# Kernel optimization log

Measured on AMD Instinct MI355X. Metric: run time of the kernel, lower is better.

The kernel has to match this reference:

```python
import jax, jax.numpy as jnp
import numpy as np

B, T, D = 16, 2048, 256

def setup_inputs() -> dict:
    key = jax.random.key(0)
    k1, k2, k3 = jax.random.split(key, 3)
    q = jax.random.normal(k1, (B, T, D), dtype=jnp.float32)
    a = jax.random.normal(k2, (B, T, D), dtype=jnp.float32)
    # original uses 'uniform' init; scale ~ small
    U = jax.random.uniform(k3, (D, D), dtype=jnp.float32, minval=-0.05, maxval=0.05)
    return {"q": q, "a": a, "U": U}

def reference(q, a, U):
    # G[b,i,j] = tanh( (q[b,i,:] @ U) . a[b,j,:] )
    qU = jnp.einsum('btd,de->bte', q, U)                 # [B,Tq,D]
    G = jnp.tanh(jnp.einsum('btd,bsd->bts', qU, a))      # [B,Tq,Ta]
    g_q = jax.nn.softmax(jnp.max(G, axis=-1), axis=1)    # [B,Tq]
    g_a = jax.nn.softmax(jnp.max(G, axis=1), axis=1)     # [B,Ta]
    q_out = jnp.einsum('btd,bt->bd', q, g_q)             # [B,D]
    a_out = jnp.einsum('bsd,bs->bd', a, g_a)             # [B,D]
    return (q_out, a_out)
```

## Files before the change

### kernel.cpp

```cpp
#include <hip/hip_runtime.h>
#include <stdint.h>

typedef __attribute__((ext_vector_type(8))) short s8v;
typedef __attribute__((ext_vector_type(4))) float f4v;

__device__ __forceinline__ unsigned short f2bf(float f) {
  unsigned u = __float_as_uint(f);
  u = u + 0x7FFFu + ((u >> 16) & 1u);
  return (unsigned short)(u >> 16);
}
__device__ __forceinline__ unsigned encf(float f) {
  unsigned i = __float_as_uint(f);
  return (i & 0x80000000u) ? ~i : (i | 0x80000000u);
}
__device__ __forceinline__ float decf(unsigned u) {
  unsigned i = (u & 0x80000000u) ? (u & 0x7FFFFFFFu) : ~u;
  return __uint_as_float(i);
}
__device__ __forceinline__ void gload_lds16(const unsigned short* g, unsigned short* l) {
  __builtin_amdgcn_global_load_lds((const __attribute__((address_space(1))) void*)g,
                                   (__attribute__((address_space(3))) void*)l, 16, 0, 0);
}

__global__ void convert_kernel(const float4* __restrict__ q, const float4* __restrict__ a,
                               const float* __restrict__ U,
                               ushort4* __restrict__ qb, ushort4* __restrict__ ab,
                               unsigned short* __restrict__ Ut,
                               unsigned* __restrict__ rcmax, float* __restrict__ out) {
  const int bx = blockIdx.x;
  if (bx < 8192) {
    const int i = bx * 256 + threadIdx.x;
    float4 v = q[i];
    qb[i] = make_ushort4(f2bf(v.x), f2bf(v.y), f2bf(v.z), f2bf(v.w));
    float4 w = a[i];
    ab[i] = make_ushort4(f2bf(w.x), f2bf(w.y), f2bf(w.z), f2bf(w.w));
  } else if (bx < 8256) {
    const int idx = (bx - 8192) * 256 + threadIdx.x;
    const int n  = idx >> 6;
    const int k4 = (idx & 63) * 4;
    ushort4 o;
    o.x = f2bf(U[(k4 + 0) * 256 + n]);
    o.y = f2bf(U[(k4 + 1) * 256 + n]);
    o.z = f2bf(U[(k4 + 2) * 256 + n]);
    o.w = f2bf(U[(k4 + 3) * 256 + n]);
    *(ushort4*)&Ut[n * 256 + k4] = o;
  } else if (bx < 8320) {
    const int idx = (bx - 8256) * 256 + threadIdx.x;
    *(uint4*)&rcmax[idx * 4] = make_uint4(0u, 0u, 0u, 0u);
  } else {
    out[(bx - 8320) * 256 + threadIdx.x] = 0.f;
  }
}

__global__ __attribute__((amdgpu_flat_work_group_size(512, 512), amdgpu_waves_per_eu(2, 2)))
void fused_qu_smax(const unsigned short* __restrict__ qb,
                   const unsigned short* __restrict__ Ut,
                   const unsigned short* __restrict__ ab,
                   unsigned* __restrict__ rowmax,
                   unsigned* __restrict__ colmax) {
  extern __shared__ char smem[];
  unsigned short* qUs    = (unsigned short*)smem;
  unsigned short* Bs2    = (unsigned short*)(smem + 65536);
  unsigned*       colLds = (unsigned*)(smem + 131072);
  unsigned*       rowLds = (unsigned*)(smem + 139264);
#define SBUF(k) ((unsigned short*)(smem + ((k) << 15)))

  const int tid = threadIdx.x;
  const int b = blockIdx.x, tm = blockIdx.y;

  const int lane = tid & 63;
  const int m16  = lane & 15;
  const int quad = lane >> 4;
  const int wave = tid >> 6;
  const int wm   = wave >> 2;
  const int wn   = wave & 3;
  const int wr32 = (wave >> 1) * 32;
  const int wc32 = (wave & 1) * 32;
  const int srow = tid >> 3;
  const int scol = (((tid & 7) ^ (srow & 7))) * 8;

  #pragma unroll
  for (int i = 0; i < 4; ++i) colLds[i * 512 + tid] = 0u;
  if (tid < 128) rowLds[tid] = 0u;

  const unsigned short* Ab_ = ab + (long)b * 2048 * 256;

#define STG64(tb, dst) do {                                                    \
    _Pragma("unroll")                                                          \
    for (int e_ = 0; e_ < 4; ++e_) {                                           \
      const int u_ = e_ * 512 + tid;         \
      const int row_ = u_ >> 5;                                                \
      const int chs_ = (u_ & 31) ^ (row_ & 7);                                 \
      gload_lds16(Ab_ + (long)((tb) * 64 + row_) * 256 + chs_ * 8,             \
                  &(dst)[u_ * 8]);                                             \
    }                                                                          \
  } while (0)

  const unsigned short* Aq = qb + ((long)b * 2048 + tm * 128) * 256;
  {
    f4v acc[4][4] = {};

#define STAGE1(kt, dst) do {                                                   \
    const int k0_ = (kt) * 64;                                                 \
    _Pragma("unroll")                                                          \
    for (int i_ = 0; i_ < 2; ++i_)                                             \
      gload_lds16(Aq + (long)(i_ * 64 + srow) * 256 + k0_ + scol,              \
                  &(dst)[i_ * 4096 + tid * 8]);                                \
    _Pragma("unroll")                                                          \
    for (int i_ = 0; i_ < 4; ++i_)                                             \
      gload_lds16(Ut + (long)(i_ * 64 + srow) * 256 + k0_ + scol,              \
                  &(dst)[8192 + i_ * 4096 + tid * 8]);                         \
  } while (0)

#define COMPUTE1(buf) do {                                                     \
    _Pragma("unroll")                                                          \
    for (int kk_ = 0; kk_ < 2; ++kk_) {                                        \
      const int cs_ = ((kk_ * 4 + quad) ^ (m16 & 7)) * 8;                      \
      s8v af_[4], bf_[4];                                                      \
      _Pragma("unroll")                                                        \
      for (int i_ = 0; i_ < 4; ++i_)                                           \
        af_[i_] = *(const s8v*)&(buf)[(wm * 64 + i_ * 16 + m16) * 64 + cs_];   \
      _Pragma("unroll")                                                        \
      for (int j_ = 0; j_ < 4; ++j_)                                           \
        bf_[j_] = *(const s8v*)&(buf)[8192 + (wn * 64 + j_ * 16 + m16) * 64 + cs_]; \
      _Pragma("unroll")                                                        \
      for (int i_ = 0; i_ < 4; ++i_)                                           \
        _Pragma("unroll")                                                      \
        for (int j_ = 0; j_ < 4; ++j_)                                         \
          acc[i_][j_] = __builtin_amdgcn_mfma_f32_16x16x32_bf16(af_[i_], bf_[j_], acc[i_][j_], 0, 0, 0); \
    }                                                                          \
  } while (0)

    STAGE1(0, Bs2);
    STAGE1(1, qUs);
    asm volatile("s_waitcnt vmcnt(6)" ::: "memory");
    __builtin_amdgcn_s_barrier();
    COMPUTE1(Bs2);
    __builtin_amdgcn_s_barrier();
    STAGE1(2, Bs2);
    asm volatile("s_waitcnt vmcnt(6)" ::: "memory");
    __builtin_amdgcn_s_barrier();
    COMPUTE1(qUs);
    __builtin_amdgcn_s_barrier();
    STAGE1(3, qUs);
    asm volatile("s_waitcnt vmcnt(6)" ::: "memory");
    __builtin_amdgcn_s_barrier();
    COMPUTE1(Bs2);
    asm volatile("s_waitcnt vmcnt(0)" ::: "memory");
    __builtin_amdgcn_s_barrier();
    STG64(0, SBUF(2));
    STG64(1, SBUF(3));
    COMPUTE1(qUs);
    asm volatile("s_waitcnt lgkmcnt(0)" ::: "memory");
    __builtin_amdgcn_s_barrier();

    #pragma unroll
    for (int i = 0; i < 4; ++i)
      #pragma unroll
      for (int r = 0; r < 4; ++r) {
        const int lr = wm * 64 + i * 16 + quad * 4 + r;
        #pragma unroll
        for (int j = 0; j < 4; ++j) {
          const int col = wn * 64 + j * 16 + m16;
          const int ch = (col >> 3) ^ (lr & 7);
          qUs[lr * 256 + ch * 8 + (col & 7)] = f2bf(acc[i][j][r]);
        }
      }
  }
  asm volatile("s_waitcnt lgkmcnt(0)" ::: "memory");
  __builtin_amdgcn_s_barrier();

  s8v aq[2][8];
  #pragma unroll
  for (int kq = 0; kq < 8; ++kq) {
    const int cs = ((kq * 4 + quad) ^ (m16 & 7)) * 8;
    aq[0][kq] = *(const s8v*)&qUs[(wr32 + m16) * 256 + cs];
    aq[1][kq] = *(const s8v*)&qUs[(wr32 + 16 + m16) * 256 + cs];
  }
  asm volatile("s_waitcnt lgkmcnt(0)" ::: "memory");
  __builtin_amdgcn_s_barrier();
  STG64(2, SBUF(0));

  float rmx[2][4];
  #pragma unroll
  for (int i = 0; i < 2; ++i)
    #pragma unroll
    for (int r = 0; r < 4; ++r) rmx[i][r] = -3.4e38f;

#define CMP64(tb, buf) do {                                                    \
    f4v acc[2][2] = {};                                                        \
    _Pragma("unroll")                                                          \
    for (int kq_ = 0; kq_ < 8; ++kq_) {                                        \
      const int cs_ = ((kq_ * 4 + quad) ^ (m16 & 7)) * 8;                      \
      _Pragma("unroll")                                                        \
      for (int j_ = 0; j_ < 2; ++j_) {                                         \
        const s8v bv_ = *(const s8v*)&(buf)[(wc32 + j_ * 16 + m16) * 256 + cs_]; \
        acc[0][j_] = __builtin_amdgcn_mfma_f32_16x16x32_bf16(aq[0][kq_], bv_, acc[0][j_], 0, 0, 0); \
        acc[1][j_] = __builtin_amdgcn_mfma_f32_16x16x32_bf16(aq[1][kq_], bv_, acc[1][j_], 0, 0, 0); \
      }                                                                        \
    }                                                                          \
    _Pragma("unroll")                                                          \
    for (int i_ = 0; i_ < 2; ++i_)                                             \
      _Pragma("unroll")                                                        \
      for (int r_ = 0; r_ < 4; ++r_)                                           \
        rmx[i_][r_] = fmaxf(rmx[i_][r_], fmaxf(acc[i_][0][r_], acc[i_][1][r_])); \
    _Pragma("unroll")                                                          \
    for (int j_ = 0; j_ < 2; ++j_) {                                           \
      float v_ = fmaxf(fmaxf(acc[0][j_][0], acc[0][j_][1]),                    \
                       fmaxf(acc[0][j_][2], acc[0][j_][3]));                   \
      v_ = fmaxf(v_, fmaxf(fmaxf(acc[1][j_][0], acc[1][j_][1]),                \
                           fmaxf(acc[1][j_][2], acc[1][j_][3])));              \
      v_ = fmaxf(v_, __shfl_xor(v_, 16));                                      \
      v_ = fmaxf(v_, __shfl_xor(v_, 32));                                      \
      if (quad == 0)                                                           \
        atomicMax(&colLds[(tb) * 64 + wc32 + j_ * 16 + m16], encf(v_));        \
    }                                                                          \
  } while (0)

  #pragma unroll 1
  for (int t = 0; t < 30; ++t) {
    asm volatile("s_waitcnt vmcnt(8)" ::: "memory");
    __builtin_amdgcn_s_barrier();
    if (t <= 28) STG64(t + 3, SBUF((t + 1) & 3));
    CMP64(t, SBUF((t + 2) & 3));
    __builtin_amdgcn_s_barrier();
  }
  asm volatile("s_waitcnt vmcnt(4)" ::: "memory");
  __builtin_amdgcn_s_barrier();
  CMP64(30, SBUF(0));
  __builtin_amdgcn_s_barrier();
  asm volatile("s_waitcnt vmcnt(0)" ::: "memory");
  __builtin_amdgcn_s_barrier();
  CMP64(31, SBUF(1));

  #pragma unroll
  for (int i = 0; i < 2; ++i)
    #pragma unroll
    for (int r = 0; r < 4; ++r) {
      float v = rmx[i][r];
      #pragma unroll
      for (int d2 = 1; d2 < 16; d2 <<= 1) v = fmaxf(v, __shfl_xor(v, d2));
      if (m16 == 0) atomicMax(&rowLds[wr32 + i * 16 + quad * 4 + r], encf(v));
    }
  __syncthreads();
  if (tid < 128)
    rowmax[(long)b * 2048 + tm * 128 + tid] = rowLds[tid];
  #pragma unroll
  for (int i = 0; i < 4; ++i)
    atomicMax(&colmax[(long)b * 2048 + i * 512 + tid], colLds[i * 512 + tid]);
}

__global__ void wsum_kernel(const uint4* __restrict__ qb, const uint4* __restrict__ ab,
                            const unsigned* __restrict__ rowmax, const unsigned* __restrict__ colmax,
                            float* __restrict__ out) {
  const int tid = threadIdx.x;
  const int chunk = blockIdx.x;
  const int b = blockIdx.y;
  const int z = blockIdx.z;
  const unsigned* e = z ? colmax : rowmax;
  const uint4* src = z ? ab : qb;

  __shared__ float sm[4];
  __shared__ float ss[4];
  __shared__ float wLds[128];
  __shared__ float red[256 * 8];

  float x[8];
  float m = -3.4e38f;
  #pragma unroll
  for (int j = 0; j < 8; ++j) {
    x[j] = tanhf(decf(e[b * 2048 + j * 256 + tid]));
    m = fmaxf(m, x[j]);
  }
  #pragma unroll
  for (int d2 = 1; d2 < 64; d2 <<= 1) m = fmaxf(m, __shfl_xor(m, d2));
  if ((tid & 63) == 0) sm[tid >> 6] = m;
  __syncthreads();
  m = fmaxf(fmaxf(sm[0], sm[1]), fmaxf(sm[2], sm[3]));
  float s = 0.f;
  #pragma unroll
  for (int j = 0; j < 8; ++j) s += expf(x[j] - m);
  #pragma unroll
  for (int d2 = 1; d2 < 64; d2 <<= 1) s += __shfl_xor(s, d2);
  if ((tid & 63) == 0) ss[tid >> 6] = s;
  __syncthreads();
  const float inv = 1.f / (ss[0] + ss[1] + ss[2] + ss[3]);

  if (tid < 128) {
    float xv = tanhf(decf(e[b * 2048 + chunk * 128 + tid]));
    wLds[tid] = expf(xv - m) * inv;
  }
  __syncthreads();

  const int dg = tid & 31;
  const int rg = tid >> 5;
  float acc[8] = {};
  const long rowbase = (long)b * 2048 + chunk * 128;
  for (int t = rg; t < 128; t += 8) {
    const float wgt = wLds[t];
    uint4 v = src[(rowbase + t) * 32 + dg];
    acc[0] += wgt * __uint_as_float(v.x << 16);
    acc[1] += wgt * __uint_as_float(v.x & 0xFFFF0000u);
    acc[2] += wgt * __uint_as_float(v.y << 16);
    acc[3] += wgt * __uint_as_float(v.y & 0xFFFF0000u);
    acc[4] += wgt * __uint_as_float(v.z << 16);
    acc[5] += wgt * __uint_as_float(v.z & 0xFFFF0000u);
    acc[6] += wgt * __uint_as_float(v.w << 16);
    acc[7] += wgt * __uint_as_float(v.w & 0xFFFF0000u);
  }
  #pragma unroll
  for (int k = 0; k < 8; ++k) red[tid * 8 + k] = acc[k];
  __syncthreads();
  if (tid < 32) {
    #pragma unroll
    for (int k = 0; k < 8; ++k) {
      float v = 0.f;
      #pragma unroll
      for (int g = 0; g < 8; ++g) v += red[((g << 5) | tid) * 8 + k];
      atomicAdd(&out[z * 4096 + b * 256 + tid * 8 + k], v);
    }
  }
}

extern "C" void kernel_launch(void* const* d_in, const int* in_sizes, int n_in,
                              void* d_out, int out_size, void* d_ws, size_t ws_size,
                              hipStream_t stream) {
  const float* q = (const float*)d_in[0];
  const float* a = (const float*)d_in[1];
  const float* U = (const float*)d_in[2];
  float* out = (float*)d_out;

  char* w = (char*)d_ws;
  unsigned short* qb = (unsigned short*)w;
  unsigned short* ab = (unsigned short*)(w + (16ull << 20));
  unsigned short* Ut = (unsigned short*)(w + (32ull << 20));
  unsigned* rmax = (unsigned*)(w + (32ull << 20) + (128ull << 10));
  unsigned* cmax = rmax + 32768;

  constexpr int SMEM = 139776;
  hipFuncSetAttribute((const void*)fused_qu_smax,
                      hipFuncAttributeMaxDynamicSharedMemorySize, SMEM);

  convert_kernel<<<8352, 256, 0, stream>>>((const float4*)q, (const float4*)a, U,
                                           (ushort4*)qb, (ushort4*)ab, Ut, rmax, out);

  fused_qu_smax<<<dim3(16, 16), 512, SMEM, stream>>>(qb, Ut, ab, rmax, cmax);

  wsum_kernel<<<dim3(16, 16, 2), 256, 0, stream>>>((const uint4*)qb, (const uint4*)ab,
                                                   rmax, cmax, out);
}
```

Before: 156.4 us.

## Retile score GEMM to 64x16 per wave with qU fragments held in AGPRs

Each wave now covers 64 query rows by 16 key columns instead of 32x32. This halves the per-wave LDS reads of the streamed key tile, loading each B fragment once and reusing it across four MFMAs. To hold the doubled A-operand (qU) fragments, they are parked in accumulation registers via inline v_accvgpr_write and read back before each MFMA. The price is extra accvgpr read instructions and s_nop padding inside the inner loop, plus inline asm that limits the compiler's scheduling.

```diff
diff --git a/kernel.cpp b/kernel.cpp
--- a/kernel.cpp
+++ b/kernel.cpp
@@ -20,6 +20,9 @@
 __device__ __forceinline__ void gload_lds16(const unsigned short* g, unsigned short* l) {
   __builtin_amdgcn_global_load_lds((const __attribute__((address_space(1))) void*)g,
                                    (__attribute__((address_space(3))) void*)l, 16, 0, 0);
+}
+__device__ __forceinline__ s8v u4s8(uint4 d) {
+  union { uint4 u; s8v s; } x; x.u = d; return x.s;
 }
 
 __global__ void convert_kernel(const float4* __restrict__ q, const float4* __restrict__ a,
@@ -74,8 +77,7 @@
   const int wave = tid >> 6;
   const int wm   = wave >> 2;
   const int wn   = wave & 3;
-  const int wr32 = (wave >> 1) * 32;
-  const int wc32 = (wave & 1) * 32;
+  const int wc16 = wn * 16;
   const int srow = tid >> 3;
   const int scol = (((tid & 7) ^ (srow & 7))) * 8;
 
@@ -170,51 +172,107 @@
   asm volatile("s_waitcnt lgkmcnt(0)" ::: "memory");
   __builtin_amdgcn_s_barrier();
 
-  s8v aq[2][8];
-  #pragma unroll
-  for (int kq = 0; kq < 8; ++kq) {
-    const int cs = ((kq * 4 + quad) ^ (m16 & 7)) * 8;
-    aq[0][kq] = *(const s8v*)&qUs[(wr32 + m16) * 256 + cs];
-    aq[1][kq] = *(const s8v*)&qUs[(wr32 + 16 + m16) * 256 + cs];
-  }
+  unsigned aqr[4][8][4];
+
+#define AQW(I, KQ) do {                                                        \
+    uint4 t_ = *(const uint4*)&qUs[(wm * 64 + (I) * 16 + m16) * 256 +          \
+                                   (((KQ) * 4 + quad) ^ (m16 & 7)) * 8];       \
+    asm volatile("v_accvgpr_write_b32 %0, %4\n\t"                              \
+                 "v_accvgpr_write_b32 %1, %5\n\t"                              \
+                 "v_accvgpr_write_b32 %2, %6\n\t"                              \
+                 "v_accvgpr_write_b32 %3, %7"                                  \
+                 : "=a"(aqr[I][KQ][0]), "=a"(aqr[I][KQ][1]),                   \
+                   "=a"(aqr[I][KQ][2]), "=a"(aqr[I][KQ][3])                    \
+                 : "v"(t_.x), "v"(t_.y), "v"(t_.z), "v"(t_.w));                \
+  } while (0)
+
+#define AQR(I, KQ, D)                                                          \
+    asm volatile("v_accvgpr_read_b32 %0, %4\n\t"                               \
+                 "v_accvgpr_read_b32 %1, %5\n\t"                               \
+                 "v_accvgpr_read_b32 %2, %6\n\t"                               \
+                 "v_accvgpr_read_b32 %3, %7\n\t"                               \
+                 "s_nop 1"                                                     \
+                 : "=v"((D).x), "=v"((D).y), "=v"((D).z), "=v"((D).w)          \
+                 : "a"(aqr[I][KQ][0]), "a"(aqr[I][KQ][1]),                     \
+                   "a"(aqr[I][KQ][2]), "a"(aqr[I][KQ][3]))
+
+#define MF(D, BV, C) __builtin_amdgcn_mfma_f32_16x16x32_bf16(u4s8(D), (BV), (C), 0, 0, 0)
+
+  AQW(0, 0); AQW(0, 1); AQW(0, 2); AQW(0, 3);
+  AQW(0, 4); AQW(0, 5); AQW(0, 6); AQW(0, 7);
+  AQW(1, 0); AQW(1, 1); AQW(1, 2); AQW(1, 3);
+  AQW(1, 4); AQW(1, 5); AQW(1, 6); AQW(1, 7);
+  AQW(2, 0); AQW(2, 1); AQW(2, 2); AQW(2, 3);
+  AQW(2, 4); AQW(2, 5); AQW(2, 6); AQW(2, 7);
+  AQW(3, 0); AQW(3, 1); AQW(3, 2); AQW(3, 3);
+  AQW(3, 4); AQW(3, 5); AQW(3, 6); AQW(3, 7);
   asm volatile("s_waitcnt lgkmcnt(0)" ::: "memory");
   __builtin_amdgcn_s_barrier();
   STG64(2, SBUF(0));
 
-  float rmx[2][4];
-  #pragma unroll
-  for (int i = 0; i < 2; ++i)
+  float rmx[4][4];
+  #pragma unroll
+  for (int i = 0; i < 4; ++i)
     #pragma unroll
     for (int r = 0; r < 4; ++r) rmx[i][r] = -3.4e38f;
 
 #define CMP64(tb, buf) do {                                                    \
-    f4v acc[2][2] = {};                                                        \
+    f4v c0 = {}, c1 = {}, c2 = {}, c3 = {};                                    \
+    const unsigned short* bp_ = &(buf)[(wc16 + m16) * 256];                    \
+    const s8v bv0 = *(const s8v*)&bp_[((0 * 4 + quad) ^ (m16 & 7)) * 8];       \
+    const s8v bv1 = *(const s8v*)&bp_[((1 * 4 + quad) ^ (m16 & 7)) * 8];       \
+    const s8v bv2 = *(const s8v*)&bp_[((2 * 4 + quad) ^ (m16 & 7)) * 8];       \
+    const s8v bv3 = *(const s8v*)&bp_[((3 * 4 + quad) ^ (m16 & 7)) * 8];       \
+    const s8v bv4 = *(const s8v*)&bp_[((4 * 4 + quad) ^ (m16 & 7)) * 8];       \
+    const s8v bv5 = *(const s8v*)&bp_[((5 * 4 + quad) ^ (m16 & 7)) * 8];       \
+    const s8v bv6 = *(const s8v*)&bp_[((6 * 4 + quad) ^ (m16 & 7)) * 8];       \
+    const s8v bv7 = *(const s8v*)&bp_[((7 * 4 + quad) ^ (m16 & 7)) * 8];       \
+    { uint4 d_; AQR(0, 0, d_); c0 = MF(d_, bv0, c0); }                         \
+    { uint4 d_; AQR(1, 0, d_); c1 = MF(d_, bv0, c1); }                         \
+    { uint4 d_; AQR(2, 0, d_); c2 = MF(d_, bv0, c2); }                         \
+    { uint4 d_; AQR(3, 0, d_); c3 = MF(d_, bv0, c3); }                         \
+    { uint4 d_; AQR(0, 1, d_); c0 = MF(d_, bv1, c0); }                         \
+    { uint4 d_; AQR(1, 1, d_); c1 = MF(d_, bv1, c1); }                         \
+    { uint4 d_; AQR(2, 1, d_); c2 = MF(d_, bv1, c2); }                         \
+    { uint4 d_; AQR(3, 1, d_); c3 = MF(d_, bv1, c3); }                         \
+    { uint4 d_; AQR(0, 2, d_); c0 = MF(d_, bv2, c0); }                         \
+    { uint4 d_; AQR(1, 2, d_); c1 = MF(d_, bv2, c1); }                         \
+    { uint4 d_; AQR(2, 2, d_); c2 = MF(d_, bv2, c2); }                         \
+    { uint4 d_; AQR(3, 2, d_); c3 = MF(d_, bv2, c3); }                         \
+    { uint4 d_; AQR(0, 3, d_); c0 = MF(d_, bv3, c0); }                         \
+    { uint4 d_; AQR(1, 3, d_); c1 = MF(d_, bv3, c1); }                         \
+    { uint4 d_; AQR(2, 3, d_); c2 = MF(d_, bv3, c2); }                         \
+    { uint4 d_; AQR(3, 3, d_); c3 = MF(d_, bv3, c3); }                         \
+    { uint4 d_; AQR(0, 4, d_); c0 = MF(d_, bv4, c0); }                         \
+    { uint4 d_; AQR(1, 4, d_); c1 = MF(d_, bv4, c1); }                         \
+    { uint4 d_; AQR(2, 4, d_); c2 = MF(d_, bv4, c2); }                         \
+    { uint4 d_; AQR(3, 4, d_); c3 = MF(d_, bv4, c3); }                         \
+    { uint4 d_; AQR(0, 5, d_); c0 = MF(d_, bv5, c0); }                         \
+    { uint4 d_; AQR(1, 5, d_); c1 = MF(d_, bv5, c1); }                         \
+    { uint4 d_; AQR(2, 5, d_); c2 = MF(d_, bv5, c2); }                         \
+    { uint4 d_; AQR(3, 5, d_); c3 = MF(d_, bv5, c3); }                         \
+    { uint4 d_; AQR(0, 6, d_); c0 = MF(d_, bv6, c0); }                         \
+    { uint4 d_; AQR(1, 6, d_); c1 = MF(d_, bv6, c1); }                         \
+    { uint4 d_; AQR(2, 6, d_); c2 = MF(d_, bv6, c2); }                         \
+    { uint4 d_; AQR(3, 6, d_); c3 = MF(d_, bv6, c3); }                         \
+    { uint4 d_; AQR(0, 7, d_); c0 = MF(d_, bv7, c0); }                         \
+    { uint4 d_; AQR(1, 7, d_); c1 = MF(d_, bv7, c1); }                         \
+    { uint4 d_; AQR(2, 7, d_); c2 = MF(d_, bv7, c2); }                         \
+    { uint4 d_; AQR(3, 7, d_); c3 = MF(d_, bv7, c3); }                         \
     _Pragma("unroll")                                                          \
-    for (int kq_ = 0; kq_ < 8; ++kq_) {                                        \
-      const int cs_ = ((kq_ * 4 + quad) ^ (m16 & 7)) * 8;                      \
-      _Pragma("unroll")                                                        \
-      for (int j_ = 0; j_ < 2; ++j_) {                                         \
-        const s8v bv_ = *(const s8v*)&(buf)[(wc32 + j_ * 16 + m16) * 256 + cs_]; \
-        acc[0][j_] = __builtin_amdgcn_mfma_f32_16x16x32_bf16(aq[0][kq_], bv_, acc[0][j_], 0, 0, 0); \
-        acc[1][j_] = __builtin_amdgcn_mfma_f32_16x16x32_bf16(aq[1][kq_], bv_, acc[1][j_], 0, 0, 0); \
-      }                                                                        \
+    for (int r_ = 0; r_ < 4; ++r_) {                                           \
+      rmx[0][r_] = fmaxf(rmx[0][r_], c0[r_]);                                  \
+      rmx[1][r_] = fmaxf(rmx[1][r_], c1[r_]);                                  \
+      rmx[2][r_] = fmaxf(rmx[2][r_], c2[r_]);                                  \
+      rmx[3][r_] = fmaxf(rmx[3][r_], c3[r_]);                                  \
     }                                                                          \
-    _Pragma("unroll")                                                          \
-    for (int i_ = 0; i_ < 2; ++i_)                                             \
-      _Pragma("unroll")                                                        \
-      for (int r_ = 0; r_ < 4; ++r_)                                           \
-        rmx[i_][r_] = fmaxf(rmx[i_][r_], fmaxf(acc[i_][0][r_], acc[i_][1][r_])); \
-    _Pragma("unroll")                                                          \
-    for (int j_ = 0; j_ < 2; ++j_) {                                           \
-      float v_ = fmaxf(fmaxf(acc[0][j_][0], acc[0][j_][1]),                    \
-                       fmaxf(acc[0][j_][2], acc[0][j_][3]));                   \
-      v_ = fmaxf(v_, fmaxf(fmaxf(acc[1][j_][0], acc[1][j_][1]),                \
-                           fmaxf(acc[1][j_][2], acc[1][j_][3])));              \
-      v_ = fmaxf(v_, __shfl_xor(v_, 16));                                      \
-      v_ = fmaxf(v_, __shfl_xor(v_, 32));                                      \
-      if (quad == 0)                                                           \
-        atomicMax(&colLds[(tb) * 64 + wc32 + j_ * 16 + m16], encf(v_));        \
-    }                                                                          \
+    float v_ = fmaxf(fmaxf(fmaxf(c0[0], c0[1]), fmaxf(c0[2], c0[3])),          \
+                     fmaxf(fmaxf(c1[0], c1[1]), fmaxf(c1[2], c1[3])));         \
+    v_ = fmaxf(v_, fmaxf(fmaxf(fmaxf(c2[0], c2[1]), fmaxf(c2[2], c2[3])),      \
+                         fmaxf(fmaxf(c3[0], c3[1]), fmaxf(c3[2], c3[3]))));    \
+    v_ = fmaxf(v_, __shfl_xor(v_, 16));                                        \
+    v_ = fmaxf(v_, __shfl_xor(v_, 32));                                        \
+    if (quad == 0) atomicMax(&colLds[(tb) * 64 + wc16 + m16], encf(v_));       \
   } while (0)
 
   #pragma unroll 1
@@ -234,13 +292,13 @@
   CMP64(31, SBUF(1));
 
   #pragma unroll
-  for (int i = 0; i < 2; ++i)
+  for (int i = 0; i < 4; ++i)
     #pragma unroll
     for (int r = 0; r < 4; ++r) {
       float v = rmx[i][r];
       #pragma unroll
       for (int d2 = 1; d2 < 16; d2 <<= 1) v = fmaxf(v, __shfl_xor(v, d2));
-      if (m16 == 0) atomicMax(&rowLds[wr32 + i * 16 + quad * 4 + r], encf(v));
+      if (m16 == 0) atomicMax(&rowLds[wm * 64 + i * 16 + quad * 4 + r], encf(v));
     }
   __syncthreads();
   if (tid < 128)
```

Result: slower. 171.6 us (+9.7%).

## Retile score GEMM to 64x16 per wave with A operand held in AGPRs

Applied to the files above, without the earlier changes.

Each wave's output tile of the score matrix changes from 32x32 to 64 rows by 16 columns. The full 64x256 qU slice now stays resident in accumulation registers (AGPRs), fed through inline-asm MFMA with an 'a' constraint. Each wave now reads only one 16-column B strip from shared memory per tile instead of two, which halves LDS traffic for the streamed A operand. It also cuts the column-max atomics to one per lane-group. In exchange, register pressure rises sharply from 128 AGPR dwords for qU. Hand-written asm with manual s_nop hazard padding is fragile and may restrict the compiler's scheduling.

```diff
diff --git a/kernel.cpp b/kernel.cpp
--- a/kernel.cpp
+++ b/kernel.cpp
@@ -3,6 +3,7 @@
 
 typedef __attribute__((ext_vector_type(8))) short s8v;
 typedef __attribute__((ext_vector_type(4))) float f4v;
+typedef __attribute__((ext_vector_type(4))) unsigned u4v;
 
 __device__ __forceinline__ unsigned short f2bf(float f) {
   unsigned u = __float_as_uint(f);
@@ -74,8 +75,7 @@
   const int wave = tid >> 6;
   const int wm   = wave >> 2;
   const int wn   = wave & 3;
-  const int wr32 = (wave >> 1) * 32;
-  const int wc32 = (wave & 1) * 32;
+  const int wc16 = wn * 16;
   const int srow = tid >> 3;
   const int scol = (((tid & 7) ^ (srow & 7))) * 8;
 
@@ -170,51 +170,63 @@
   asm volatile("s_waitcnt lgkmcnt(0)" ::: "memory");
   __builtin_amdgcn_s_barrier();
 
-  s8v aq[2][8];
-  #pragma unroll
-  for (int kq = 0; kq < 8; ++kq) {
-    const int cs = ((kq * 4 + quad) ^ (m16 & 7)) * 8;
-    aq[0][kq] = *(const s8v*)&qUs[(wr32 + m16) * 256 + cs];
-    aq[1][kq] = *(const s8v*)&qUs[(wr32 + 16 + m16) * 256 + cs];
-  }
+  u4v aqf[4][8];
+  #pragma unroll
+  for (int i = 0; i < 4; ++i)
+    #pragma unroll
+    for (int kq = 0; kq < 8; ++kq)
+      aqf[i][kq] = *(const u4v*)&qUs[(wm * 64 + i * 16 + m16) * 256 +
+                                     ((kq * 4 + quad) ^ (m16 & 7)) * 8];
   asm volatile("s_waitcnt lgkmcnt(0)" ::: "memory");
   __builtin_amdgcn_s_barrier();
   STG64(2, SBUF(0));
 
-  float rmx[2][4];
-  #pragma unroll
-  for (int i = 0; i < 2; ++i)
+  float rmx[4][4];
+  #pragma unroll
+  for (int i = 0; i < 4; ++i)
     #pragma unroll
     for (int r = 0; r < 4; ++r) rmx[i][r] = -3.4e38f;
 
+#define MFA(I, KQ, BV, C)                                                      \
+    asm("v_mfma_f32_16x16x32_bf16 %0, %1, %2, %0"                              \
+        : "+v"(C) : "a"(aqf[I][KQ]), "v"(BV))
+
 #define CMP64(tb, buf) do {                                                    \
-    f4v acc[2][2] = {};                                                        \
-    _Pragma("unroll")                                                          \
-    for (int kq_ = 0; kq_ < 8; ++kq_) {                                        \
-      const int cs_ = ((kq_ * 4 + quad) ^ (m16 & 7)) * 8;                      \
-      _Pragma("unroll")                                                        \
-      for (int j_ = 0; j_ < 2; ++j_) {                                         \
-        const s8v bv_ = *(const s8v*)&(buf)[(wc32 + j_ * 16 + m16) * 256 + cs_]; \
-        acc[0][j_] = __builtin_amdgcn_mfma_f32_16x16x32_bf16(aq[0][kq_], bv_, acc[0][j_], 0, 0, 0); \
-        acc[1][j_] = __builtin_amdgcn_mfma_f32_16x16x32_bf16(aq[1][kq_], bv_, acc[1][j_], 0, 0, 0); \
-      }                                                                        \
+    f4v c0 = {}, c1 = {}, c2 = {}, c3 = {};                                    \
+    const unsigned short* bp_ = &(buf)[(wc16 + m16) * 256];                    \
+    const s8v bv0 = *(const s8v*)&bp_[((0 * 4 + quad) ^ (m16 & 7)) * 8];       \
+    const s8v bv1 = *(const s8v*)&bp_[((1 * 4 + quad) ^ (m16 & 7)) * 8];       \
+    const s8v bv2 = *(const s8v*)&bp_[((2 * 4 + quad) ^ (m16 & 7)) * 8];       \
+    const s8v bv3 = *(const s8v*)&bp_[((3 * 4 + quad) ^ (m16 & 7)) * 8];       \
+    const s8v bv4 = *(const s8v*)&bp_[((4 * 4 + quad) ^ (m16 & 7)) * 8];       \
+    const s8v bv5 = *(const s8v*)&bp_[((5 * 4 + quad) ^ (m16 & 7)) * 8];       \
+    const s8v bv6 = *(const s8v*)&bp_[((6 * 4 + quad) ^ (m16 & 7)) * 8];       \
+    const s8v bv7 = *(const s8v*)&bp_[((7 * 4 + quad) ^ (m16 & 7)) * 8];       \
+    MFA(0, 0, bv0, c0); MFA(1, 0, bv0, c1); MFA(2, 0, bv0, c2); MFA(3, 0, bv0, c3); \
+    MFA(0, 1, bv1, c0); MFA(1, 1, bv1, c1); MFA(2, 1, bv1, c2); MFA(3, 1, bv1, c3); \
+    MFA(0, 2, bv2, c0); MFA(1, 2, bv2, c1); MFA(2, 2, bv2, c2); MFA(3, 2, bv2, c3); \
+    MFA(0, 3, bv3, c0); MFA(1, 3, bv3, c1); MFA(2, 3, bv3, c2); MFA(3, 3, bv3, c3); \
+    MFA(0, 4, bv4, c0); MFA(1, 4, bv4, c1); MFA(2, 4, bv4, c2); MFA(3, 4, bv4, c3); \
+    MFA(0, 5, bv5, c0); MFA(1, 5, bv5, c1); MFA(2, 5, bv5, c2); MFA(3, 5, bv5, c3); \
+    MFA(0, 6, bv6, c0); MFA(1, 6, bv6, c1); MFA(2, 6, bv6, c2); MFA(3, 6, bv6, c3); \
+    MFA(0, 7, bv7, c0); MFA(1, 7, bv7, c1); MFA(2, 7, bv7, c2); MFA(3, 7, bv7, c3); \
+      \
+       \
+    asm volatile("s_nop 7\n\ts_nop 7" :::);                                    \
+    _Pragma("unroll")                                                          \
+    for (int r_ = 0; r_ < 4; ++r_) {                                           \
+      rmx[0][r_] = fmaxf(rmx[0][r_], c0[r_]);                                  \
+      rmx[1][r_] = fmaxf(rmx[1][r_], c1[r_]);                                  \
+      rmx[2][r_] = fmaxf(rmx[2][r_], c2[r_]);                                  \
+      rmx[3][r_] = fmaxf(rmx[3][r_], c3[r_]);                                  \
     }                                                                          \
-    _Pragma("unroll")                                                          \
-    for (int i_ = 0; i_ < 2; ++i_)                                             \
-      _Pragma("unroll")                                                        \
-      for (int r_ = 0; r_ < 4; ++r_)                                           \
-        rmx[i_][r_] = fmaxf(rmx[i_][r_], fmaxf(acc[i_][0][r_], acc[i_][1][r_])); \
-    _Pragma("unroll")                                                          \
-    for (int j_ = 0; j_ < 2; ++j_) {                                           \
-      float v_ = fmaxf(fmaxf(acc[0][j_][0], acc[0][j_][1]),                    \
-                       fmaxf(acc[0][j_][2], acc[0][j_][3]));                   \
-      v_ = fmaxf(v_, fmaxf(fmaxf(acc[1][j_][0], acc[1][j_][1]),                \
-                           fmaxf(acc[1][j_][2], acc[1][j_][3])));              \
-      v_ = fmaxf(v_, __shfl_xor(v_, 16));                                      \
-      v_ = fmaxf(v_, __shfl_xor(v_, 32));                                      \
-      if (quad == 0)                                                           \
-        atomicMax(&colLds[(tb) * 64 + wc32 + j_ * 16 + m16], encf(v_));        \
-    }                                                                          \
+    float v_ = fmaxf(fmaxf(fmaxf(c0[0], c0[1]), fmaxf(c0[2], c0[3])),          \
+                     fmaxf(fmaxf(c1[0], c1[1]), fmaxf(c1[2], c1[3])));         \
+    v_ = fmaxf(v_, fmaxf(fmaxf(fmaxf(c2[0], c2[1]), fmaxf(c2[2], c2[3])),      \
+                         fmaxf(fmaxf(c3[0], c3[1]), fmaxf(c3[2], c3[3]))));    \
+    v_ = fmaxf(v_, __shfl_xor(v_, 16));                                        \
+    v_ = fmaxf(v_, __shfl_xor(v_, 32));                                        \
+    if (quad == 0) atomicMax(&colLds[(tb) * 64 + wc16 + m16], encf(v_));       \
   } while (0)
 
   #pragma unroll 1
@@ -234,13 +246,13 @@
   CMP64(31, SBUF(1));
 
   #pragma unroll
-  for (int i = 0; i < 2; ++i)
+  for (int i = 0; i < 4; ++i)
     #pragma unroll
     for (int r = 0; r < 4; ++r) {
       float v = rmx[i][r];
       #pragma unroll
       for (int d2 = 1; d2 < 16; d2 <<= 1) v = fmaxf(v, __shfl_xor(v, d2));
-      if (m16 == 0) atomicMax(&rowLds[wr32 + i * 16 + quad * 4 + r], encf(v));
+      if (m16 == 0) atomicMax(&rowLds[wm * 64 + i * 16 + quad * 4 + r], encf(v));
     }
   __syncthreads();
   if (tid < 128)
```

Result: no change. 156.6 us (+0.1%).
